# Performance work log

Measured on AMD Instinct MI355X. Metric: run time of the kernel, lower is better.

Reference implementation:

```python
import jax, jax.numpy as jnp
import numpy as np
from jax import lax

# 4th-order Butterworth lowpass, scipy.signal.butter(4, 0.2)
B_COEF = np.array([0.004824343357716228, 0.019297373430864913, 0.02894606014629737,
                   0.019297373430864913, 0.004824343357716228], dtype=np.float32)
A_COEF = np.array([1.0, -2.369513007182038, 2.3139884144006453,
                   -1.0546654058785672, 0.18737949236818502], dtype=np.float32)


def setup_inputs() -> dict:
    key = jax.random.key(0)
    x = jax.random.normal(key, (8, 64, 48000), dtype=jnp.float32)
    return {"x": x, "b": jnp.asarray(B_COEF), "a": jnp.asarray(A_COEF)}


def _pad_odd(x, n):
    # Faithful to torch _pad_odd (including its exact slicing on the right side).
    left = 2.0 * x[..., 0:1] - jnp.flip(x[..., 0:n], axis=-1)
    right = 2.0 * x[..., -1:] - jnp.flip(x[..., -(n + 2):-2], axis=-1)
    return jnp.concatenate([left, x, right], axis=-1)


def _lfilter(x, a, b):
    # y[n] = (sum_k b[k] x[n-k] - sum_j a[j] y[n-j]) / a[0]
    a0 = a[0]
    bn = b / a0
    an = a[1:] / a0                      # [N], N = order
    ntaps = b.shape[0]                   # static
    N = a.shape[0] - 1                   # static
    T = x.shape[-1]
    # FIR part: small static tap loop, fully vectorized over batch/time.
    pad = [(0, 0)] * (x.ndim - 1) + [(ntaps - 1, 0)]
    xp = jnp.pad(x, pad)
    f = bn[0] * xp[..., ntaps - 1: ntaps - 1 + T]
    for k in range(1, ntaps):
        f = f + bn[k] * xp[..., ntaps - 1 - k: ntaps - 1 - k + T]
    # IIR recurrence via scan over time.
    f_t = jnp.moveaxis(f, -1, 0)         # [T, B, C]
    init = jnp.zeros(x.shape[:-1] + (N,), x.dtype)  # [B, C, N], y[t-1..t-N]

    def step(carry, ft):
        y = ft - jnp.einsum('k,...k->...', an, carry)
        carry = jnp.concatenate([y[..., None], carry[..., :-1]], axis=-1)
        return carry, y

    _, ys = lax.scan(step, init, f_t)
    return jnp.moveaxis(ys, 0, -1)       # [B, C, T]


def _filtfilt(x, a, b):
    y = _lfilter(x, a, b)
    return jnp.flip(_lfilter(jnp.flip(y, axis=-1), a, b), axis=-1)


def reference(x, b, a):
    scale = jnp.max(jnp.abs(x), axis=-1, keepdims=True)
    xs = x / scale
    padlen = 3 * max(int(a.shape[0]), int(b.shape[0]))  # 15, static
    xp = _pad_odd(xs, padlen)
    y = _filtfilt(xp, a, b)
    y = y[..., padlen:-padlen]
    return y * scale
```

## Files before the change

### kernel.cpp

```cpp
#include <hip/hip_runtime.h>


#define T48 48000
#define TP0 48030
#define LCH 48
#define NCH 1024
#define UF  13344

__device__ __forceinline__ float fget(const float4& v, int e) {
  switch (e & 3) { case 0: return v.x; case 1: return v.y; case 2: return v.z; default: return v.w; }
}

__global__ __launch_bounds__(1024, 4) void filtfilt_k(
    const float* __restrict__ x, const float* __restrict__ bco,
    const float* __restrict__ aco, float* __restrict__ out)
{
  __shared__ __align__(16) float U[UF];
  __shared__ float P[10][16];

  const int c = threadIdx.x;
  const float* __restrict__ xs = x + (size_t)blockIdx.x * T48;
  const float4* __restrict__ xs4 = reinterpret_cast<const float4*>(xs);
  float* __restrict__ os = out + (size_t)blockIdx.x * T48;
  float4* __restrict__ os4 = reinterpret_cast<float4*>(os);
  float4* __restrict__ U4 = reinterpret_cast<float4*>(U);

  const float inva0 = 1.f / aco[0];
  const float b0 = bco[0]*inva0, b1 = bco[1]*inva0, b2 = bco[2]*inva0,
              b3 = bco[3]*inva0, b4 = bco[4]*inva0;
  const float na1 = -aco[1]*inva0, na2 = -aco[2]*inva0,
              na3 = -aco[3]*inva0, na4 = -aco[4]*inva0;

  float4 R[4];
#pragma unroll
  for (int j = 0; j < 4; j++) {
    int g = 1024*j + c;
    if (g < 3074) { int m = min(max(g - 5, 0), 11999); R[j] = xs4[m]; }
  }

  if (c < 64) {
    const int i = (c >> 2) & 3, j = c & 3;
    float r1 = (j==0)?1.f:0.f, r2 = (j==1)?1.f:0.f,
          r3 = (j==2)?1.f:0.f, r4 = (j==3)?1.f:0.f;
#pragma unroll
    for (int n = 0; n < LCH; n++) {
      float h = fmaf(na1, r1, fmaf(na2, r2, fmaf(na3, r3, na4 * r4)));
      r4 = r3; r3 = r2; r2 = r1; r1 = h;
    }
    float c0 = __shfl(r1, j), c1 = __shfl(r2, j),
          c2 = __shfl(r3, j), c3 = __shfl(r4, j);
    float Pv = (i==0)?c0 : (i==1)?c1 : (i==2)?c2 : c3;
    if (c < 16) P[0][c] = Pv;
#pragma unroll
    for (int k = 0; k < 9; k++) {
      float rA0 = __shfl(Pv, i*4+0), rA1 = __shfl(Pv, i*4+1),
            rA2 = __shfl(Pv, i*4+2), rA3 = __shfl(Pv, i*4+3);
      float cB0 = __shfl(Pv, 0*4+j), cB1 = __shfl(Pv, 1*4+j),
            cB2 = __shfl(Pv, 2*4+j), cB3 = __shfl(Pv, 3*4+j);
      Pv = rA0*cB0 + rA1*cB1 + rA2*cB2 + rA3*cB3;
      if (c < 16) P[k+1][c] = Pv;
    }
  }

  float w4v, w3v, w2v, w1v;
  float A[LCH];
  for (int s = 0; s < 4; s++) {
    __syncthreads();
#pragma unroll
    for (int j = 0; j < 4; j++) {
      int g = 1024*j + c;
      if (g < 3074) {
        float4 v = R[j];
        bool slow = (s == 0 && g <= 4) || (s == 3 && g >= 2789);
        if (slow) {
          float x0d = 2.f * xs[0], xld = 2.f * xs[T48-1];
#pragma unroll
          for (int e = 0; e < 4; e++) {
            int p = 12288*s - 5 + 4*g + e;
            float vv = 0.f;
            if (s == 0) { if (p >= 0) vv = x0d - xs[14 - p]; }
            else        { if (p < TP0) vv = xld - xs[96012 - p]; }
            if (e == 0) v.x = vv; else if (e == 1) v.y = vv;
            else if (e == 2) v.z = vv; else v.w = vv;
          }
        }
        U4[g + g/12] = v;
      }
    }
    if (s < 3) {
#pragma unroll
      for (int j = 0; j < 4; j++) {
        int g = 1024*j + c;
        if (g < 3074) { int m = min(max(3072*(s+1) - 5 + g, 0), 11999); R[j] = xs4[m]; }
      }
    }
    __syncthreads();
    if ((c >> 8) == s) {
      const int cl = c & 255;
      float4 F[14];
#pragma unroll
      for (int k = 0; k < 14; k++)
        F[k] = U4[13*cl + k + (k >= 12 ? 1 : 0)];
      w4v = F[0].y; w3v = F[0].z; w2v = F[0].w; w1v = F[1].x;
#pragma unroll
      for (int n = 0; n < LCH; n++) A[n] = fget(F[(n + 5) >> 2], (n + 5) & 3);
    }
  }
  __syncthreads();

  float r1 = 0.f, r2 = 0.f, r3 = 0.f, r4 = 0.f;
#pragma unroll
  for (int n = 0; n < LCH; n++) {
    float xv = A[n];
    float f = fmaf(b0,xv, fmaf(b1,w1v, fmaf(b2,w2v, fmaf(b3,w3v, b4*w4v))));
    w4v = w3v; w3v = w2v; w2v = w1v; w1v = xv;
    float u = fmaf(na4, r4, f);
    u = fmaf(na3, r3, u); u = fmaf(na2, r2, u); u = fmaf(na1, r1, u);
    A[n] = u; r4 = r3; r3 = r2; r2 = r1; r1 = u;
  }

  float4* Sb0 = U4;
  float4* Sb1 = U4 + 1024;
  Sb0[c] = make_float4(r1, r2, r3, r4);
  __syncthreads();
#pragma unroll
  for (int k = 0; k < 10; k++) {
    float4* cur = (k & 1) ? Sb1 : Sb0;
    float4* nxt = (k & 1) ? Sb0 : Sb1;
    const int off = 1 << k;
    float4 t = cur[c];
    if (c >= off) {
      float4 q = cur[c - off];
      t.x += P[k][0]*q.x  + P[k][1]*q.y  + P[k][2]*q.z  + P[k][3]*q.w;
      t.y += P[k][4]*q.x  + P[k][5]*q.y  + P[k][6]*q.z  + P[k][7]*q.w;
      t.z += P[k][8]*q.x  + P[k][9]*q.y  + P[k][10]*q.z + P[k][11]*q.w;
      t.w += P[k][12]*q.x + P[k][13]*q.y + P[k][14]*q.z + P[k][15]*q.w;
    }
    nxt[c] = t;
    __syncthreads();
  }
  float4 sv = make_float4(0.f,0.f,0.f,0.f);
  if (c > 0) sv = Sb0[c-1];

  {
    float h1 = sv.x, h2 = sv.y, h3 = sv.z, h4 = sv.w;
#pragma unroll
    for (int n = 0; n < LCH; n++) {
      float h = fmaf(na1, h1, fmaf(na2, h2, fmaf(na3, h3, na4 * h4)));
      A[n] += h;
      h4 = h3; h3 = h2; h2 = h1; h1 = h;
    }
  }
  if (c >= 1000) {
#pragma unroll
    for (int n = 0; n < LCH; n++) if (48*c + n >= TP0) A[n] = 0.f;
  }

  Sb1[c] = make_float4(A[0], A[1], A[2], A[3]);
  __syncthreads();
  float h0 = 0.f, h1v = 0.f, h2v = 0.f, h3v = 0.f;
  if (c < NCH - 1) { float4 hv = Sb1[c+1]; h0 = hv.x; h1v = hv.y; h2v = hv.z; h3v = hv.w; }

#define YV(i) ((i) < 48 ? A[(i)] : ((i)==48 ? h0 : (i)==49 ? h1v : (i)==50 ? h2v : h3v))
  r1 = 0.f; r2 = 0.f; r3 = 0.f; r4 = 0.f;
#pragma unroll
  for (int m = 0; m < LCH; m++) {
    float g = fmaf(b0, YV(47-m), fmaf(b1, YV(48-m),
              fmaf(b2, YV(49-m), fmaf(b3, YV(50-m), b4 * YV(51-m)))));
    float u = fmaf(na4, r4, g);
    u = fmaf(na3, r3, u); u = fmaf(na2, r2, u); u = fmaf(na1, r1, u);
    r4 = r3; r3 = r2; r2 = r1; r1 = u;
    if      (m == 0) h3v = u;
    else if (m == 1) h2v = u;
    else if (m == 2) h1v = u;
    else if (m == 3) h0  = u;
    else             A[51 - m] = u;
  }
#undef YV

  const int d = NCH - 1 - c;
  Sb0[d] = make_float4(r1, r2, r3, r4);
  __syncthreads();
#pragma unroll
  for (int k = 0; k < 10; k++) {
    float4* cur = (k & 1) ? Sb1 : Sb0;
    float4* nxt = (k & 1) ? Sb0 : Sb1;
    const int off = 1 << k;
    float4 t = cur[d];
    if (d >= off) {
      float4 q = cur[d - off];
      t.x += P[k][0]*q.x  + P[k][1]*q.y  + P[k][2]*q.z  + P[k][3]*q.w;
      t.y += P[k][4]*q.x  + P[k][5]*q.y  + P[k][6]*q.z  + P[k][7]*q.w;
      t.z += P[k][8]*q.x  + P[k][9]*q.y  + P[k][10]*q.z + P[k][11]*q.w;
      t.w += P[k][12]*q.x + P[k][13]*q.y + P[k][14]*q.z + P[k][15]*q.w;
    }
    nxt[d] = t;
    __syncthreads();
  }
  float4 ev = make_float4(0.f,0.f,0.f,0.f);
  if (d > 0) ev = Sb0[d-1];

  {
    float g1 = ev.x, g2 = ev.y, g3 = ev.z, g4 = ev.w;
#pragma unroll
    for (int m = 0; m < LCH; m++) {
      float h = fmaf(na1, g1, fmaf(na2, g2, fmaf(na3, g3, na4 * g4)));
      if      (m == 0) h3v += h;
      else if (m == 1) h2v += h;
      else if (m == 2) h1v += h;
      else if (m == 3) h0  += h;
      else             A[51 - m] += h;
      g4 = g3; g3 = g2; g2 = g1; g1 = h;
    }
  }

  __syncthreads();
  for (int s = 0; s < 4; s++) {
#pragma unroll
    for (int k4 = 0; k4 < 12; k4++) {
      int u4 = 12*c - 3 + k4;
      unsigned lu4 = (unsigned)(u4 - 3000*s);
      if (lu4 <= 3000u) {
        float4 v;
        if (k4 < 11) v = make_float4(A[4*k4+4], A[4*k4+5], A[4*k4+6], A[4*k4+7]);
        else         v = make_float4(h0, h1v, h2v, h3v);
        U4[(int)lu4 + (int)lu4/12] = v;
      }
    }
    __syncthreads();
#pragma unroll
    for (int j = 0; j < 3; j++) {
      int t4l = 1024*j + c;
      if (t4l < 3000) {
        int q0 = t4l, q1 = t4l + 1;
        int a0 = 4*(q0 + q0/12) + 3;
        int bi = 4*(q1 + q1/12);
        float4 v;
        v.x = U[a0]; v.y = U[bi]; v.z = U[bi+1]; v.w = U[bi+2];
        os4[3000*s + t4l] = v;
      }
    }
    __syncthreads();
  }
}

extern "C" void kernel_launch(void* const* d_in, const int* in_sizes, int n_in,
                              void* d_out, int out_size, void* d_ws, size_t ws_size,
                              hipStream_t stream) {
  (void)n_in; (void)d_ws; (void)ws_size; (void)out_size;
  const float* x = (const float*)d_in[0];
  const float* b = (const float*)d_in[1];
  const float* a = (const float*)d_in[2];
  float* out = (float*)d_out;
  const int nseq = in_sizes[0] / T48;
  filtfilt_k<<<dim3(nseq), dim3(1024), 0, stream>>>(x, b, a, out);
}
```

Before: 204.6 us.

## Replace block-wide LDS scans with hierarchical wave-shuffle scans and per-wave staging

The block-level 10-step LDS scan of IIR carry states, which needed a __syncthreads per step, becomes a hierarchical scan: a 6-step intra-wave shuffle scan, one block barrier, and a 16-entry inter-wave scan done with shuffles. Input loading and output transposition move from block-wide staged phases to per-wave private LDS slices synchronized only by wave barriers. Together these cut block barriers and LDS traffic, at the cost of extra shuffle arithmetic and more complex boundary handling, including direct scalar stores for edge samples.

New measurement: 229.4 us. 12.1% more time.

```diff
diff --git a/kernel.cpp b/kernel.cpp
--- a/kernel.cpp
+++ b/kernel.cpp
@@ -3,27 +3,27 @@
 
 #define T48 48000
 #define TP0 48030
-#define LCH 48
-#define NCH 1024
-#define UF  13344
-
-__device__ __forceinline__ float fget(const float4& v, int e) {
-  switch (e & 3) { case 0: return v.x; case 1: return v.y; case 2: return v.z; default: return v.w; }
-}
+#define SLICE4 108
+#define HZ_OFF 40
+#define WA_OFF 56
+#define WB_OFF 72
+#define SL_OFF 88
+#define LDS_F4 (88 + 16 * SLICE4)
 
 __global__ __launch_bounds__(1024, 4) void filtfilt_k(
     const float* __restrict__ x, const float* __restrict__ bco,
     const float* __restrict__ aco, float* __restrict__ out)
 {
-  __shared__ __align__(16) float U[UF];
-  __shared__ float P[10][16];
-
-  const int c = threadIdx.x;
-  const float* __restrict__ xs = x + (size_t)blockIdx.x * T48;
+  __shared__ __align__(16) float4 LS[LDS_F4];
+  float* LSf = reinterpret_cast<float*>(LS);
+
+  const int c  = threadIdx.x;
+  const int w  = c >> 6;
+  const int ln = c & 63;
+  const float* __restrict__ xs  = x + (size_t)blockIdx.x * T48;
   const float4* __restrict__ xs4 = reinterpret_cast<const float4*>(xs);
   float* __restrict__ os = out + (size_t)blockIdx.x * T48;
   float4* __restrict__ os4 = reinterpret_cast<float4*>(os);
-  float4* __restrict__ U4 = reinterpret_cast<float4*>(U);
 
   const float inva0 = 1.f / aco[0];
   const float b0 = bco[0]*inva0, b1 = bco[1]*inva0, b2 = bco[2]*inva0,
@@ -31,26 +31,17 @@
   const float na1 = -aco[1]*inva0, na2 = -aco[2]*inva0,
               na3 = -aco[3]*inva0, na4 = -aco[4]*inva0;
 
-  float4 R[4];
-#pragma unroll
-  for (int j = 0; j < 4; j++) {
-    int g = 1024*j + c;
-    if (g < 3074) { int m = min(max(g - 5, 0), 11999); R[j] = xs4[m]; }
-  }
-
-  if (c < 64) {
-    const int i = (c >> 2) & 3, j = c & 3;
+  {
+    const int j = ln & 3, i = (ln >> 2) & 3;
     float r1 = (j==0)?1.f:0.f, r2 = (j==1)?1.f:0.f,
           r3 = (j==2)?1.f:0.f, r4 = (j==3)?1.f:0.f;
 #pragma unroll
-    for (int n = 0; n < LCH; n++) {
+    for (int n = 0; n < 48; n++) {
       float h = fmaf(na1, r1, fmaf(na2, r2, fmaf(na3, r3, na4 * r4)));
       r4 = r3; r3 = r2; r2 = r1; r1 = h;
     }
-    float c0 = __shfl(r1, j), c1 = __shfl(r2, j),
-          c2 = __shfl(r3, j), c3 = __shfl(r4, j);
-    float Pv = (i==0)?c0 : (i==1)?c1 : (i==2)?c2 : c3;
-    if (c < 16) P[0][c] = Pv;
+    float Pv = (i==0)?r1 : (i==1)?r2 : (i==2)?r3 : r4;
+    if (ln < 16) LSf[ln] = Pv;
 #pragma unroll
     for (int k = 0; k < 9; k++) {
       float rA0 = __shfl(Pv, i*4+0), rA1 = __shfl(Pv, i*4+1),
@@ -58,59 +49,59 @@
       float cB0 = __shfl(Pv, 0*4+j), cB1 = __shfl(Pv, 1*4+j),
             cB2 = __shfl(Pv, 2*4+j), cB3 = __shfl(Pv, 3*4+j);
       Pv = rA0*cB0 + rA1*cB1 + rA2*cB2 + rA3*cB3;
-      if (c < 16) P[k+1][c] = Pv;
-    }
-  }
-
-  float w4v, w3v, w2v, w1v;
-  float A[LCH];
-  for (int s = 0; s < 4; s++) {
-    __syncthreads();
-#pragma unroll
-    for (int j = 0; j < 4; j++) {
-      int g = 1024*j + c;
-      if (g < 3074) {
-        float4 v = R[j];
-        bool slow = (s == 0 && g <= 4) || (s == 3 && g >= 2789);
-        if (slow) {
-          float x0d = 2.f * xs[0], xld = 2.f * xs[T48-1];
+      if (ln < 16) LSf[16*(k+1) + ln] = Pv;
+    }
+  }
+
+  float A[48];
+  float w1v = 0.f, w2v = 0.f, w3v = 0.f, w4v = 0.f;
+  const int sb4 = SL_OFF + w * SLICE4;
+  for (int r = 0; r < 8; r++) {
+    asm volatile("s_waitcnt lgkmcnt(0)" ::: "memory");
+    __builtin_amdgcn_wave_barrier();
+    const int c0 = 64*w + 8*r;
+    const int G0 = 12*c0 - 5;
+    if (G0 >= 0 && G0 <= 11902) {
+      LS[sb4 + ln + ln/12] = xs4[G0 + ln];
+      if (ln < 34) { int g = 64 + ln; LS[sb4 + g + g/12] = xs4[G0 + g]; }
+    } else {
+#pragma unroll
+      for (int t = 0; t < 2; t++) {
+        int g = 64*t + ln;
+        if (g < 98) {
+          float vv[4];
 #pragma unroll
           for (int e = 0; e < 4; e++) {
-            int p = 12288*s - 5 + 4*g + e;
-            float vv = 0.f;
-            if (s == 0) { if (p >= 0) vv = x0d - xs[14 - p]; }
-            else        { if (p < TP0) vv = xld - xs[96012 - p]; }
-            if (e == 0) v.x = vv; else if (e == 1) v.y = vv;
-            else if (e == 2) v.z = vv; else v.w = vv;
+            int q = 4*(G0 + g) + e;
+            float v = 0.f;
+            if (q >= 0 && q < T48)      v = xs[q];
+            else if (q < 0)             { if (q >= -15) v = 2.f*xs[0] - xs[-1 - q]; }
+            else                        { if (q < T48 + 15) v = 2.f*xs[T48-1] - xs[2*T48 - 3 - q]; }
+            vv[e] = v;
           }
+          LS[sb4 + g + g/12] = make_float4(vv[0], vv[1], vv[2], vv[3]);
         }
-        U4[g + g/12] = v;
-      }
-    }
-    if (s < 3) {
-#pragma unroll
-      for (int j = 0; j < 4; j++) {
-        int g = 1024*j + c;
-        if (g < 3074) { int m = min(max(3072*(s+1) - 5 + g, 0), 11999); R[j] = xs4[m]; }
-      }
-    }
-    __syncthreads();
-    if ((c >> 8) == s) {
-      const int cl = c & 255;
-      float4 F[14];
-#pragma unroll
-      for (int k = 0; k < 14; k++)
-        F[k] = U4[13*cl + k + (k >= 12 ? 1 : 0)];
-      w4v = F[0].y; w3v = F[0].z; w2v = F[0].w; w1v = F[1].x;
-#pragma unroll
-      for (int n = 0; n < LCH; n++) A[n] = fget(F[(n + 5) >> 2], (n + 5) & 3);
-    }
-  }
-  __syncthreads();
+      }
+    }
+    asm volatile("s_waitcnt lgkmcnt(0)" ::: "memory");
+    __builtin_amdgcn_wave_barrier();
+    if ((ln >> 3) == r) {
+      const int eb = sb4 + 13*(ln & 7);
+      float4 f;
+      f = LS[eb+0];  w4v = f.y; w3v = f.z; w2v = f.w;
+      f = LS[eb+1];  w1v = f.x; A[0] = f.y; A[1] = f.z; A[2] = f.w;
+#pragma unroll
+      for (int k = 2; k <= 12; k++) {
+        f = LS[eb + k + (k >= 12 ? 1 : 0)];
+        A[4*k-5] = f.x; A[4*k-4] = f.y; A[4*k-3] = f.z; A[4*k-2] = f.w;
+      }
+      f = LS[eb+14]; A[47] = f.x;
+    }
+  }
 
   float r1 = 0.f, r2 = 0.f, r3 = 0.f, r4 = 0.f;
 #pragma unroll
-  for (int n = 0; n < LCH; n++) {
+  for (int n = 0; n < 48; n++) {
     float xv = A[n];
     float f = fmaf(b0,xv, fmaf(b1,w1v, fmaf(b2,w2v, fmaf(b3,w3v, b4*w4v))));
     w4v = w3v; w3v = w2v; w2v = w1v; w1v = xv;
@@ -118,34 +109,74 @@
     u = fmaf(na3, r3, u); u = fmaf(na2, r2, u); u = fmaf(na1, r1, u);
     A[n] = u; r4 = r3; r3 = r2; r2 = r1; r1 = u;
   }
-
-  float4* Sb0 = U4;
-  float4* Sb1 = U4 + 1024;
-  Sb0[c] = make_float4(r1, r2, r3, r4);
+  const float e0 = A[0], e1 = A[1], e2 = A[2], e3 = A[3];
+  float o1 = r1, o2 = r2, o3 = r3, o4 = r4;
+
+#pragma unroll
+  for (int k = 0; k < 6; k++) {
+    const float4 Pa = LS[4*k+0], Pb = LS[4*k+1], Pc = LS[4*k+2], Pd = LS[4*k+3];
+    const int off = 1 << k;
+    float q1 = __shfl(r1, ln-off), q2 = __shfl(r2, ln-off),
+          q3 = __shfl(r3, ln-off), q4 = __shfl(r4, ln-off);
+    if (ln < off) { q1 = 0.f; q2 = 0.f; q3 = 0.f; q4 = 0.f; }
+    r1 += Pa.x*q1 + Pa.y*q2 + Pa.z*q3 + Pa.w*q4;
+    r2 += Pb.x*q1 + Pb.y*q2 + Pb.z*q3 + Pb.w*q4;
+    r3 += Pc.x*q1 + Pc.y*q2 + Pc.z*q3 + Pc.w*q4;
+    r4 += Pd.x*q1 + Pd.y*q2 + Pd.z*q3 + Pd.w*q4;
+  }
+  if (ln == 63) LS[WA_OFF + w] = make_float4(r1, r2, r3, r4);
+  if (ln == 0)  LS[HZ_OFF + w] = make_float4(e0, e1, e2, e3);
   __syncthreads();
-#pragma unroll
-  for (int k = 0; k < 10; k++) {
-    float4* cur = (k & 1) ? Sb1 : Sb0;
-    float4* nxt = (k & 1) ? Sb0 : Sb1;
+
+  float W1 = 0.f, W2 = 0.f, W3 = 0.f, W4 = 0.f;
+  {
+    float4 Ag = LS[WA_OFF + (ln & 15)];
+    float t1 = Ag.x, t2 = Ag.y, t3 = Ag.z, t4 = Ag.w;
+#pragma unroll
+    for (int k = 0; k < 4; k++) {
+      const float4 Pa = LS[4*(6+k)+0], Pb = LS[4*(6+k)+1],
+                   Pc = LS[4*(6+k)+2], Pd = LS[4*(6+k)+3];
+      const int off = 1 << k;
+      float q1 = __shfl(t1, ln-off), q2 = __shfl(t2, ln-off),
+            q3 = __shfl(t3, ln-off), q4 = __shfl(t4, ln-off);
+      if (ln < off) { q1 = 0.f; q2 = 0.f; q3 = 0.f; q4 = 0.f; }
+      t1 += Pa.x*q1 + Pa.y*q2 + Pa.z*q3 + Pa.w*q4;
+      t2 += Pb.x*q1 + Pb.y*q2 + Pb.z*q3 + Pb.w*q4;
+      t3 += Pc.x*q1 + Pc.y*q2 + Pc.z*q3 + Pc.w*q4;
+      t4 += Pd.x*q1 + Pd.y*q2 + Pd.z*q3 + Pd.w*q4;
+    }
+    if (w > 0) { W1 = __shfl(t1, w-1); W2 = __shfl(t2, w-1);
+                 W3 = __shfl(t3, w-1); W4 = __shfl(t4, w-1); }
+  }
+  {
+    const float4 Pa = LS[0], Pb = LS[1], Pc = LS[2], Pd = LS[3];
+    float i1 = Pa.x*W1 + Pa.y*W2 + Pa.z*W3 + Pa.w*W4;
+    float i2 = Pb.x*W1 + Pb.y*W2 + Pb.z*W3 + Pb.w*W4;
+    float i3 = Pc.x*W1 + Pc.y*W2 + Pc.z*W3 + Pc.w*W4;
+    float i4 = Pd.x*W1 + Pd.y*W2 + Pd.z*W3 + Pd.w*W4;
+    r1 = o1 + (ln==0 ? i1 : 0.f); r2 = o2 + (ln==0 ? i2 : 0.f);
+    r3 = o3 + (ln==0 ? i3 : 0.f); r4 = o4 + (ln==0 ? i4 : 0.f);
+  }
+#pragma unroll
+  for (int k = 0; k < 6; k++) {
+    const float4 Pa = LS[4*k+0], Pb = LS[4*k+1], Pc = LS[4*k+2], Pd = LS[4*k+3];
     const int off = 1 << k;
-    float4 t = cur[c];
-    if (c >= off) {
-      float4 q = cur[c - off];
-      t.x += P[k][0]*q.x  + P[k][1]*q.y  + P[k][2]*q.z  + P[k][3]*q.w;
-      t.y += P[k][4]*q.x  + P[k][5]*q.y  + P[k][6]*q.z  + P[k][7]*q.w;
-      t.z += P[k][8]*q.x  + P[k][9]*q.y  + P[k][10]*q.z + P[k][11]*q.w;
-      t.w += P[k][12]*q.x + P[k][13]*q.y + P[k][14]*q.z + P[k][15]*q.w;
-    }
-    nxt[c] = t;
-    __syncthreads();
-  }
-  float4 sv = make_float4(0.f,0.f,0.f,0.f);
-  if (c > 0) sv = Sb0[c-1];
-
-  {
-    float h1 = sv.x, h2 = sv.y, h3 = sv.z, h4 = sv.w;
-#pragma unroll
-    for (int n = 0; n < LCH; n++) {
+    float q1 = __shfl(r1, ln-off), q2 = __shfl(r2, ln-off),
+          q3 = __shfl(r3, ln-off), q4 = __shfl(r4, ln-off);
+    if (ln < off) { q1 = 0.f; q2 = 0.f; q3 = 0.f; q4 = 0.f; }
+    r1 += Pa.x*q1 + Pa.y*q2 + Pa.z*q3 + Pa.w*q4;
+    r2 += Pb.x*q1 + Pb.y*q2 + Pb.z*q3 + Pb.w*q4;
+    r3 += Pc.x*q1 + Pc.y*q2 + Pc.z*q3 + Pc.w*q4;
+    r4 += Pd.x*q1 + Pd.y*q2 + Pd.z*q3 + Pd.w*q4;
+  }
+  float s1 = __shfl(r1, ln-1), s2 = __shfl(r2, ln-1),
+        s3 = __shfl(r3, ln-1), s4 = __shfl(r4, ln-1);
+  if (ln == 0) { s1 = W1; s2 = W2; s3 = W3; s4 = W4; }
+
+  {
+    float h1 = s1, h2 = s2, h3 = s3, h4 = s4;
+#pragma unroll
+    for (int n = 0; n < 48; n++) {
       float h = fmaf(na1, h1, fmaf(na2, h2, fmaf(na3, h3, na4 * h4)));
       A[n] += h;
       h4 = h3; h3 = h2; h2 = h1; h1 = h;
@@ -153,18 +184,29 @@
   }
   if (c >= 1000) {
 #pragma unroll
-    for (int n = 0; n < LCH; n++) if (48*c + n >= TP0) A[n] = 0.f;
-  }
-
-  Sb1[c] = make_float4(A[0], A[1], A[2], A[3]);
-  __syncthreads();
-  float h0 = 0.f, h1v = 0.f, h2v = 0.f, h3v = 0.f;
-  if (c < NCH - 1) { float4 hv = Sb1[c+1]; h0 = hv.x; h1v = hv.y; h2v = hv.z; h3v = hv.w; }
+    for (int n = 0; n < 48; n++) if (48*c + n >= TP0) A[n] = 0.f;
+  }
+
+  float y0n = __shfl(e0, ln+1), y1n = __shfl(e1, ln+1),
+        y2n = __shfl(e2, ln+1), y3n = __shfl(e3, ln+1);
+  if (ln == 63) {
+    float4 hz = (w < 15) ? LS[HZ_OFF + w + 1] : make_float4(0.f,0.f,0.f,0.f);
+    y0n = hz.x; y1n = hz.y; y2n = hz.z; y3n = hz.w;
+  }
+  float h0, h1v, h2v, h3v;
+  {
+    float g1 = r1, g2 = r2, g3 = r3, g4 = r4, hh;
+    hh = fmaf(na1,g1, fmaf(na2,g2, fmaf(na3,g3, na4*g4))); h0  = y0n + hh; g4=g3; g3=g2; g2=g1; g1=hh;
+    hh = fmaf(na1,g1, fmaf(na2,g2, fmaf(na3,g3, na4*g4))); h1v = y1n + hh; g4=g3; g3=g2; g2=g1; g1=hh;
+    hh = fmaf(na1,g1, fmaf(na2,g2, fmaf(na3,g3, na4*g4))); h2v = y2n + hh; g4=g3; g3=g2; g2=g1; g1=hh;
+    hh = fmaf(na1,g1, fmaf(na2,g2, fmaf(na3,g3, na4*g4))); h3v = y3n + hh;
+  }
+  if (c >= 1000) { h0 = 0.f; h1v = 0.f; h2v = 0.f; h3v = 0.f; }
 
 #define YV(i) ((i) < 48 ? A[(i)] : ((i)==48 ? h0 : (i)==49 ? h1v : (i)==50 ? h2v : h3v))
   r1 = 0.f; r2 = 0.f; r3 = 0.f; r4 = 0.f;
 #pragma unroll
-  for (int m = 0; m < LCH; m++) {
+  for (int m = 0; m < 48; m++) {
     float g = fmaf(b0, YV(47-m), fmaf(b1, YV(48-m),
               fmaf(b2, YV(49-m), fmaf(b3, YV(50-m), b4 * YV(51-m)))));
     float u = fmaf(na4, r4, g);
@@ -177,33 +219,73 @@
     else             A[51 - m] = u;
   }
 #undef YV
-
-  const int d = NCH - 1 - c;
-  Sb0[d] = make_float4(r1, r2, r3, r4);
+  o1 = r1; o2 = r2; o3 = r3; o4 = r4;
+
+#pragma unroll
+  for (int k = 0; k < 6; k++) {
+    const float4 Pa = LS[4*k+0], Pb = LS[4*k+1], Pc = LS[4*k+2], Pd = LS[4*k+3];
+    const int off = 1 << k;
+    float q1 = __shfl(r1, ln+off), q2 = __shfl(r2, ln+off),
+          q3 = __shfl(r3, ln+off), q4 = __shfl(r4, ln+off);
+    if (ln > 63 - off) { q1 = 0.f; q2 = 0.f; q3 = 0.f; q4 = 0.f; }
+    r1 += Pa.x*q1 + Pa.y*q2 + Pa.z*q3 + Pa.w*q4;
+    r2 += Pb.x*q1 + Pb.y*q2 + Pb.z*q3 + Pb.w*q4;
+    r3 += Pc.x*q1 + Pc.y*q2 + Pc.z*q3 + Pc.w*q4;
+    r4 += Pd.x*q1 + Pd.y*q2 + Pd.z*q3 + Pd.w*q4;
+  }
+  if (ln == 0) LS[WB_OFF + (15 - w)] = make_float4(r1, r2, r3, r4);
   __syncthreads();
-#pragma unroll
-  for (int k = 0; k < 10; k++) {
-    float4* cur = (k & 1) ? Sb1 : Sb0;
-    float4* nxt = (k & 1) ? Sb0 : Sb1;
+
+  W1 = 0.f; W2 = 0.f; W3 = 0.f; W4 = 0.f;
+  {
+    float4 Bg = LS[WB_OFF + (ln & 15)];
+    float t1 = Bg.x, t2 = Bg.y, t3 = Bg.z, t4 = Bg.w;
+#pragma unroll
+    for (int k = 0; k < 4; k++) {
+      const float4 Pa = LS[4*(6+k)+0], Pb = LS[4*(6+k)+1],
+                   Pc = LS[4*(6+k)+2], Pd = LS[4*(6+k)+3];
+      const int off = 1 << k;
+      float q1 = __shfl(t1, ln-off), q2 = __shfl(t2, ln-off),
+            q3 = __shfl(t3, ln-off), q4 = __shfl(t4, ln-off);
+      if (ln < off) { q1 = 0.f; q2 = 0.f; q3 = 0.f; q4 = 0.f; }
+      t1 += Pa.x*q1 + Pa.y*q2 + Pa.z*q3 + Pa.w*q4;
+      t2 += Pb.x*q1 + Pb.y*q2 + Pb.z*q3 + Pb.w*q4;
+      t3 += Pc.x*q1 + Pc.y*q2 + Pc.z*q3 + Pc.w*q4;
+      t4 += Pd.x*q1 + Pd.y*q2 + Pd.z*q3 + Pd.w*q4;
+    }
+    const int u = 15 - w;
+    if (u > 0) { W1 = __shfl(t1, u-1); W2 = __shfl(t2, u-1);
+                 W3 = __shfl(t3, u-1); W4 = __shfl(t4, u-1); }
+  }
+  {
+    const float4 Pa = LS[0], Pb = LS[1], Pc = LS[2], Pd = LS[3];
+    float i1 = Pa.x*W1 + Pa.y*W2 + Pa.z*W3 + Pa.w*W4;
+    float i2 = Pb.x*W1 + Pb.y*W2 + Pb.z*W3 + Pb.w*W4;
+    float i3 = Pc.x*W1 + Pc.y*W2 + Pc.z*W3 + Pc.w*W4;
+    float i4 = Pd.x*W1 + Pd.y*W2 + Pd.z*W3 + Pd.w*W4;
+    r1 = o1 + (ln==63 ? i1 : 0.f); r2 = o2 + (ln==63 ? i2 : 0.f);
+    r3 = o3 + (ln==63 ? i3 : 0.f); r4 = o4 + (ln==63 ? i4 : 0.f);
+  }
+#pragma unroll
+  for (int k = 0; k < 6; k++) {
+    const float4 Pa = LS[4*k+0], Pb = LS[4*k+1], Pc = LS[4*k+2], Pd = LS[4*k+3];
     const int off = 1 << k;
-    float4 t = cur[d];
-    if (d >= off) {
-      float4 q = cur[d - off];
-      t.x += P[k][0]*q.x  + P[k][1]*q.y  + P[k][2]*q.z  + P[k][3]*q.w;
-      t.y += P[k][4]*q.x  + P[k][5]*q.y  + P[k][6]*q.z  + P[k][7]*q.w;
-      t.z += P[k][8]*q.x  + P[k][9]*q.y  + P[k][10]*q.z + P[k][11]*q.w;
-      t.w += P[k][12]*q.x + P[k][13]*q.y + P[k][14]*q.z + P[k][15]*q.w;
-    }
-    nxt[d] = t;
-    __syncthreads();
-  }
-  float4 ev = make_float4(0.f,0.f,0.f,0.f);
-  if (d > 0) ev = Sb0[d-1];
-
-  {
-    float g1 = ev.x, g2 = ev.y, g3 = ev.z, g4 = ev.w;
-#pragma unroll
-    for (int m = 0; m < LCH; m++) {
+    float q1 = __shfl(r1, ln+off), q2 = __shfl(r2, ln+off),
+          q3 = __shfl(r3, ln+off), q4 = __shfl(r4, ln+off);
+    if (ln > 63 - off) { q1 = 0.f; q2 = 0.f; q3 = 0.f; q4 = 0.f; }
+    r1 += Pa.x*q1 + Pa.y*q2 + Pa.z*q3 + Pa.w*q4;
+    r2 += Pb.x*q1 + Pb.y*q2 + Pb.z*q3 + Pb.w*q4;
+    r3 += Pc.x*q1 + Pc.y*q2 + Pc.z*q3 + Pc.w*q4;
+    r4 += Pd.x*q1 + Pd.y*q2 + Pd.z*q3 + Pd.w*q4;
+  }
+  s1 = __shfl(r1, ln+1); s2 = __shfl(r2, ln+1);
+  s3 = __shfl(r3, ln+1); s4 = __shfl(r4, ln+1);
+  if (ln == 63) { s1 = W1; s2 = W2; s3 = W3; s4 = W4; }
+
+  {
+    float g1 = s1, g2 = s2, g3 = s3, g4 = s4;
+#pragma unroll
+    for (int m = 0; m < 48; m++) {
       float h = fmaf(na1, g1, fmaf(na2, g2, fmaf(na3, g3, na4 * g4)));
       if      (m == 0) h3v += h;
       else if (m == 1) h2v += h;
@@ -214,33 +296,50 @@
     }
   }
 
-  __syncthreads();
-  for (int s = 0; s < 4; s++) {
-#pragma unroll
-    for (int k4 = 0; k4 < 12; k4++) {
-      int u4 = 12*c - 3 + k4;
-      unsigned lu4 = (unsigned)(u4 - 3000*s);
-      if (lu4 <= 3000u) {
-        float4 v;
-        if (k4 < 11) v = make_float4(A[4*k4+4], A[4*k4+5], A[4*k4+6], A[4*k4+7]);
-        else         v = make_float4(h0, h1v, h2v, h3v);
-        U4[(int)lu4 + (int)lu4/12] = v;
-      }
-    }
-    __syncthreads();
-#pragma unroll
-    for (int j = 0; j < 3; j++) {
-      int t4l = 1024*j + c;
-      if (t4l < 3000) {
-        int q0 = t4l, q1 = t4l + 1;
-        int a0 = 4*(q0 + q0/12) + 3;
-        int bi = 4*(q1 + q1/12);
-        float4 v;
-        v.x = U[a0]; v.y = U[bi]; v.z = U[bi+1]; v.w = U[bi+2];
-        os4[3000*s + t4l] = v;
-      }
-    }
-    __syncthreads();
+  const int sbf = 4 * sb4;
+  for (int r8 = 0; r8 < 8; r8++) {
+    asm volatile("s_waitcnt lgkmcnt(0)" ::: "memory");
+    __builtin_amdgcn_wave_barrier();
+    const int c0 = 64*w + 8*r8;
+    if ((ln >> 3) == r8) {
+      const int D = ln & 7;
+      const int zb = sbf + 52*D;
+#pragma unroll
+      for (int k4 = 0; k4 < 11; k4++)
+        *reinterpret_cast<float4*>(&LSf[zb + 4*k4]) =
+            make_float4(A[4*k4+4], A[4*k4+5], A[4*k4+6], A[4*k4+7]);
+      *reinterpret_cast<float4*>(&LSf[zb + 44]) = make_float4(h0, h1v, h2v, h3v);
+      if (D == 0) {
+        int th = 48*c0 - 15;
+        if ((unsigned)(th)   < 48000u) os[th]   = A[4];
+        if ((unsigned)(th+1) < 48000u) os[th+1] = A[5];
+        if ((unsigned)(th+2) < 48000u) os[th+2] = A[6];
+      }
+      if (D == 7) {
+        int tt = 48*c0 + 368;
+        if ((unsigned)tt < 48000u) os[tt] = h3v;
+      }
+    }
+    asm volatile("s_waitcnt lgkmcnt(0)" ::: "memory");
+    __builtin_amdgcn_wave_barrier();
+#pragma unroll
+    for (int t2 = 0; t2 < 2; t2++) {
+      int g = 64*t2 + ln;
+      if (g < 95) {
+        int j4 = 12*c0 - 3 + g;
+        if ((unsigned)j4 < 12000u) {
+          int idx0 = 3 + 4*g;
+          int Dg = idx0 / 48;
+          int rem = idx0 - 48*Dg;
+          int base = sbf + 52*Dg + rem;
+          float v0 = LSf[base];
+          float v1 = LSf[base + 1 + (rem+1 >= 48 ? 4 : 0)];
+          float v2 = LSf[base + 2 + (rem+2 >= 48 ? 4 : 0)];
+          float v3 = LSf[base + 3 + (rem+3 >= 48 ? 4 : 0)];
+          os4[j4] = make_float4(v0, v1, v2, v3);
+        }
+      }
+    }
   }
 }
 
```
